# Optimization experiments

Hardware: AMD Instinct MI355X
Metric: run time of the kernel (lower is better)

## Reference

```python
import jax, jax.numpy as jnp
import numpy as np

N_NODES = 20000
N_EDGES = 320000
N_GRAPHS = 32
IN_CH = 5
HID = 64
HEADS = 4
DH = HID // HEADS  # 16
LAYERS = 8
EPS = 1e-5
SLOPE = 0.2


def setup_inputs() -> dict:
    key = jax.random.key(0)
    ks = jax.random.split(key, 32)
    inp = {}
    inp['x1'] = jax.random.normal(ks[0], (N_NODES, IN_CH), dtype=jnp.float32)
    inp['x2'] = jax.random.normal(ks[1], (N_NODES, IN_CH), dtype=jnp.float32)
    inp['edge_index1'] = jax.random.randint(ks[2], (2, N_EDGES), 0, N_NODES, dtype=jnp.int32)
    inp['edge_index2'] = jax.random.randint(ks[3], (2, N_EDGES), 0, N_NODES, dtype=jnp.int32)
    inp['batch1'] = jnp.sort(jax.random.randint(ks[4], (N_NODES,), 0, N_GRAPHS, dtype=jnp.int32))
    inp['batch2'] = jnp.sort(jax.random.randint(ks[5], (N_NODES,), 0, N_GRAPHS, dtype=jnp.int32))
    # node_lin
    inp['Wn'] = jax.random.normal(ks[6], (IN_CH, HID), dtype=jnp.float32) / np.sqrt(IN_CH)
    inp['bnode'] = jnp.zeros((HID,), dtype=jnp.float32)
    # GATv2 layers (stacked over LAYERS)
    s = 1.0 / np.sqrt(HID)
    inp['Wl'] = jax.random.normal(ks[7], (LAYERS, HID, HID), dtype=jnp.float32) * s
    inp['bl'] = jnp.zeros((LAYERS, HID), dtype=jnp.float32)
    inp['Wr'] = jax.random.normal(ks[8], (LAYERS, HID, HID), dtype=jnp.float32) * s
    inp['br'] = jnp.zeros((LAYERS, HID), dtype=jnp.float32)
    inp['att'] = jax.random.normal(ks[9], (LAYERS, HEADS, DH), dtype=jnp.float32) / np.sqrt(DH)
    inp['cbias'] = jnp.zeros((LAYERS, HID), dtype=jnp.float32)
    # batch norms
    inp['gamma'] = jnp.ones((LAYERS, HID), dtype=jnp.float32)
    inp['beta'] = jnp.zeros((LAYERS, HID), dtype=jnp.float32)
    # fc head
    inp['f1w'] = jax.random.normal(ks[10], (2 * HID, 256), dtype=jnp.float32) / np.sqrt(2 * HID)
    inp['f1b'] = jnp.zeros((256,), dtype=jnp.float32)
    inp['f2w'] = jax.random.normal(ks[11], (256, 128), dtype=jnp.float32) / np.sqrt(256)
    inp['f2b'] = jnp.zeros((128,), dtype=jnp.float32)
    inp['f3w'] = jax.random.normal(ks[12], (128, 1), dtype=jnp.float32) / np.sqrt(128)
    inp['f3b'] = jnp.zeros((1,), dtype=jnp.float32)
    return inp


def _gatv2_layer(x, src, dst, Wl, bl, Wr, br, att, bias):
    # x: [N, HID]; src/dst: [E'] (self loops included)
    N = x.shape[0]
    xl = (x @ Wl + bl).reshape(N, HEADS, DH)  # source transform
    xr = (x @ Wr + br).reshape(N, HEADS, DH)  # target transform
    e = jax.nn.leaky_relu(xl[src] + xr[dst], SLOPE)          # [E, H, DH]
    score = jnp.einsum('ehd,hd->eh', e, att)                  # [E, H]
    smax = jax.ops.segment_max(score, dst, num_segments=N)    # [N, H]
    ex = jnp.exp(score - smax[dst])
    denom = jax.ops.segment_sum(ex, dst, num_segments=N)
    alpha = ex / denom[dst]                                   # [E, H]
    msg = alpha[:, :, None] * xl[src]                         # [E, H, DH]
    out = jax.ops.segment_sum(msg, dst, num_segments=N)       # [N, H, DH]
    return out.reshape(N, HID) + bias


def _forward_once(x, edge_index, batch, Wn, bnode, Wl, bl, Wr, br, att, cbias, gamma, beta):
    N = x.shape[0]
    loop = jnp.arange(N, dtype=edge_index.dtype)
    src = jnp.concatenate([edge_index[0], loop])  # add_self_loops=True
    dst = jnp.concatenate([edge_index[1], loop])
    h = x @ Wn + bnode
    for l in range(LAYERS):
        g = _gatv2_layer(h, src, dst, Wl[l], bl[l], Wr[l], br[l], att[l], cbias[l])
        mu = g.mean(axis=0)
        var = g.var(axis=0)
        g = (g - mu) / jnp.sqrt(var + EPS) * gamma[l] + beta[l]
        h = h + jax.nn.elu(g)
    # global_mean_pool
    sums = jax.ops.segment_sum(h, batch, num_segments=N_GRAPHS)
    cnt = jax.ops.segment_sum(jnp.ones((N,), dtype=h.dtype), batch, num_segments=N_GRAPHS)
    return sums / jnp.maximum(cnt, 1.0)[:, None]


def reference(x1, edge_index1, batch1, x2, edge_index2, batch2, Wn, bnode, Wl, bl, Wr, br, att, cbias, gamma, beta, f1w, f1b, f2w, f2b, f3w, f3b):
    o1 = _forward_once(x1, edge_index1, batch1, Wn, bnode, Wl, bl, Wr, br, att, cbias, gamma, beta)
    o2 = _forward_once(x2, edge_index2, batch2, Wn, bnode, Wl, bl, Wr, br, att, cbias, gamma, beta)
    c = jnp.concatenate([o1, o2], axis=1)           # [G, 128]
    h = jax.nn.relu(c @ f1w + f1b)                   # dropout = identity (eval)
    h = jax.nn.relu(h @ f2w + f2b)
    return h @ f3w + f3b                             # [G, 1]
```

## Files before the change

### kernel.cpp

```cpp
#include <hip/hip_runtime.h>
#include <hip/hip_bf16.h>
#include <hip/hip_fp16.h>

#define N_NODES 20000
#define HID 64
#define EPS 1e-5f

typedef _Float16 h2 __attribute__((ext_vector_type(2)));

struct GP {
    const int* ei;
    const int* batch;
    const float* x;
    int* deg;
    int* cursor;
    int* csr;
    float* h;
    __half* xlh;
    __half* xrh;
    float* gb;
    float* stats;
    float* osum;
};


__global__ void k_csr_init(GP a, GP b, int n, int two) {
    int t = blockIdx.x * blockDim.x + threadIdx.x;
    if (t < n) {
        a.deg[t] = 1;
        if (two) b.deg[t] = 1;
    }
}

__global__ void k_count(GP a, GP b, int Ea, int Eb, int two) {
    int t = blockIdx.x * blockDim.x + threadIdx.x;
    if (t < Ea) atomicAdd(&a.deg[a.ei[Ea + t]], 1);
    if (two && t < Eb) atomicAdd(&b.deg[b.ei[Eb + t]], 1);
}

#define SCAN_T 1024
#define SCAN_C 20
__global__ __launch_bounds__(1024) void k_scan(GP a, GP b, int n, int totA, int totB) {
    GP g = blockIdx.x ? b : a;
    int total = blockIdx.x ? totB : totA;
    __shared__ int sd[SCAN_T];
    int t = threadIdx.x;
    int base = t * SCAN_C;
    int loc[SCAN_C];
    int s = 0;
#pragma unroll
    for (int i = 0; i < SCAN_C; ++i) {
        int idx = base + i;
        loc[i] = (idx < n) ? g.deg[idx] : 0;
        s += loc[i];
    }
    sd[t] = s;
    __syncthreads();
    for (int off = 1; off < SCAN_T; off <<= 1) {
        int v = (t >= off) ? sd[t - off] : 0;
        __syncthreads();
        sd[t] += v;
        __syncthreads();
    }
    int run = sd[t] - s;
#pragma unroll
    for (int i = 0; i < SCAN_C; ++i) {
        int idx = base + i;
        if (idx < n) { g.deg[idx] = run; g.cursor[idx] = run; run += loc[i]; }
    }
    if (t == 0) g.deg[n] = total;
}

__global__ void k_scatter(GP a, GP b, int Ea, int Eb, int n, int two) {
    int t = blockIdx.x * blockDim.x + threadIdx.x;
    if (t < Ea) {
        int s = a.ei[t], d = a.ei[Ea + t];
        a.csr[atomicAdd(&a.cursor[d], 1)] = s * 128;
    } else if (t < Ea + n) {
        int nn = t - Ea;
        a.csr[atomicAdd(&a.cursor[nn], 1)] = nn * 128;
    }
    if (two) {
        if (t < Eb) {
            int s = b.ei[t], d = b.ei[Eb + t];
            b.csr[atomicAdd(&b.cursor[d], 1)] = s * 128;
        } else if (t < Eb + n) {
            int nn = t - Eb;
            b.csr[atomicAdd(&b.cursor[nn], 1)] = nn * 128;
        }
    }
}


__global__ void k_nodelin(GP a, GP b, int nPer, const float* __restrict__ Wn,
                          const float* __restrict__ bn, int n) {
    int bid = blockIdx.x;
    GP g = a;
    if (bid >= nPer) { g = b; bid -= nPer; }
    int idx = bid * 256 + threadIdx.x;
    if (idx >= n * HID) return;
    int node = idx >> 6, c = idx & 63;
    float acc = bn[c];
#pragma unroll
    for (int k = 0; k < 5; ++k) acc += g.x[node * 5 + k] * Wn[k * HID + c];
    g.h[idx] = acc;
}


__global__ __launch_bounds__(256) void k_lin2(GP ga, GP gbp, int nPer, int n,
        const float* __restrict__ Wl, const float* __restrict__ bl,
        const float* __restrict__ Wr, const float* __restrict__ br,
        const float* __restrict__ gamma, const float* __restrict__ beta, int layer) {
    __shared__ float wls[4096], wrs[4096];
    __shared__ float hs[2048];
    int bid = blockIdx.x;
    GP g = ga;
    if (bid >= nPer) { g = gbp; bid -= nPer; }
    {
        const float4* wl4 = (const float4*)Wl;
        const float4* wr4 = (const float4*)Wr;
        float4* l4 = (float4*)wls;
        float4* r4 = (float4*)wrs;
        for (int i = threadIdx.x; i < 1024; i += 256) { l4[i] = wl4[i]; r4[i] = wr4[i]; }
    }
    int c = threadIdx.x & 63;
    int wid = threadIdx.x >> 6;
    float blv = bl[c], brv = br[c];
    float mu = 0.f, inv = 1.f, gam = 1.f, bet = 0.f;
    if (layer > 0) {
        const float* st = g.stats + (layer - 1) * 128;
        float invn = 1.0f / (float)n;
        mu = st[c] * invn;
        float var = st[64 + c] * invn - mu * mu;
        inv = rsqrtf(fmaxf(var, 0.f) + EPS);
        gam = gamma[c]; bet = beta[c];
    }
    __syncthreads();
    float* hw = &hs[wid * 512];
    const float4* hw4 = (const float4*)hw;
    for (int base = bid * 32; base < n; base += nPer * 32) {
        int nb = base + wid * 8;
        size_t off0 = (size_t)nb * 64 + c;
        float hv[8];
        if (layer > 0) {
#pragma unroll
            for (int j = 0; j < 8; ++j) {
                float gv = g.gb[off0 + j * 64];
                float ov = g.h[off0 + j * 64];
                float v = (gv - mu) * inv * gam + bet;
                v = v > 0.f ? v : expm1f(v);
                hv[j] = ov + v;
                g.h[off0 + j * 64] = hv[j];
            }
        } else {
#pragma unroll
            for (int j = 0; j < 8; ++j) hv[j] = g.h[off0 + j * 64];
        }
#pragma unroll
        for (int j = 0; j < 8; ++j) hw[j * 64 + c] = hv[j];
        float accl[8], accr[8];
#pragma unroll
        for (int j = 0; j < 8; ++j) { accl[j] = blv; accr[j] = brv; }
        for (int k4 = 0; k4 < 16; ++k4) {
            float4 hq[8];
#pragma unroll
            for (int j = 0; j < 8; ++j) hq[j] = hw4[j * 16 + k4];
#pragma unroll
            for (int kk = 0; kk < 4; ++kk) {
                float wl = wls[(k4 * 4 + kk) * 64 + c];
                float wr = wrs[(k4 * 4 + kk) * 64 + c];
#pragma unroll
                for (int j = 0; j < 8; ++j) {
                    float hx = (&hq[j].x)[kk];
                    accl[j] = fmaf(hx, wl, accl[j]);
                    accr[j] = fmaf(hx, wr, accr[j]);
                }
            }
        }
#pragma unroll
        for (int j = 0; j < 8; ++j) {
            g.xlh[off0 + j * 64] = __float2half(accl[j]);
            g.xrh[off0 + j * 64] = __float2half(accr[j]);
        }
    }
}


__device__ __forceinline__ float red8(float p) {
    p += __int_as_float(__builtin_amdgcn_update_dpp(0, __float_as_int(p), 0xB1, 0xF, 0xF, true));
    p += __int_as_float(__builtin_amdgcn_update_dpp(0, __float_as_int(p), 0x4E, 0xF, 0xF, true));
    p += __int_as_float(__builtin_amdgcn_update_dpp(0, __float_as_int(p), 0x141, 0xF, 0xF, true));
    return p;
}

__global__ __launch_bounds__(1024) void k_attn(GP ga, GP gbp, int nPer,
        const float* __restrict__ att, const float* __restrict__ cbias, int layer, int n) {
    int bid = blockIdx.x;
    GP g = (bid & 1) ? gbp : ga;
    bid >>= 1;
    int lane = threadIdx.x & 63;
    int wid = threadIdx.x >> 6;
    int hh = lane >> 5;
    int cl = lane & 31;
    int gw = bid * 16 + wid;
    int nw = nPer * 16;
    const float LOG2E = 1.44269504f;
    float a0 = att[2 * cl] * LOG2E;
    float a1 = att[2 * cl + 1] * LOG2E;
    float cb0 = cbias[2 * cl], cb1 = cbias[2 * cl + 1];
    const h2 slope = {(_Float16)0.2f, (_Float16)0.2f};
    const int* __restrict__ rowptr = g.deg;
    const int* __restrict__ csr = g.csr;
    const char* xlb = (const char*)g.xlh + (size_t)cl * 4;
    const char* xrb = (const char*)g.xrh + (size_t)cl * 4;
    float* __restrict__ gbuf = g.gb;
    float* st = g.stats + layer * 128;
    float bs0 = 0.f, bs1 = 0.f, bq0 = 0.f, bq1 = 0.f;
    for (int node = gw; node < n; node += nw) {
        int start = rowptr[node], end = rowptr[node + 1];
        h2 xrv = *(const h2*)(xrb + (size_t)node * 128);
        float sself;
        {
            h2 xs = *(const h2*)(xlb + (size_t)node * 128);
            h2 t = xs + xrv;
            h2 lk = __builtin_elementwise_max(t, t * slope);
            float sp = fmaf((float)lk.x, a0, (float)lk.y * a1);
            sself = red8(sp);
        }
        float lsum = 0.f, acc0 = 0.f, acc1 = 0.f;
        int idx = start;
        for (; idx + 8 <= end; idx += 8) {
            int off[4];
            h2 xv[4];
#pragma unroll
            for (int j = 0; j < 4; ++j) off[j] = csr[idx + 2 * j + hh];
#pragma unroll
            for (int j = 0; j < 4; ++j) xv[j] = *(const h2*)(xlb + off[j]);
#pragma unroll
            for (int j = 0; j < 4; ++j) {
                h2 t = xv[j] + xrv;
                h2 lk = __builtin_elementwise_max(t, t * slope);
                float sp = fmaf((float)lk.x, a0, (float)lk.y * a1);
                float w = exp2f(fminf(red8(sp) - sself, 110.f));
                lsum += w;
                acc0 = fmaf(w, (float)xv[j].x, acc0);
                acc1 = fmaf(w, (float)xv[j].y, acc1);
            }
        }
        for (; idx < end; idx += 2) {
            int e = idx + hh;
            bool valid = e < end;
            int off = csr[valid ? e : end - 1];
            h2 xv = *(const h2*)(xlb + off);
            h2 t = xv + xrv;
            h2 lk = __builtin_elementwise_max(t, t * slope);
            float sp = fmaf((float)lk.x, a0, (float)lk.y * a1);
            float w = exp2f(fminf(red8(sp) - sself, 110.f));
            w = valid ? w : 0.f;
            lsum += w;
            acc0 = fmaf(w, (float)xv.x, acc0);
            acc1 = fmaf(w, (float)xv.y, acc1);
        }
        lsum += __shfl_xor(lsum, 32);
        acc0 += __shfl_xor(acc0, 32);
        acc1 += __shfl_xor(acc1, 32);
        if (hh == 0) {
            float invl = 1.0f / lsum;
            float o0 = acc0 * invl + cb0;
            float o1 = acc1 * invl + cb1;
            float2 o = {o0, o1};
            *(float2*)(gbuf + (size_t)node * 64 + 2 * cl) = o;
            bs0 += o0; bs1 += o1;
            bq0 += o0 * o0; bq1 += o1 * o1;
        }
    }
    __shared__ float2 sred[1024];
    float2 z = {0.f, 0.f};
    float2 v1 = {bs0, bs1};
    sred[threadIdx.x] = (hh == 0) ? v1 : z;
    __syncthreads();
    if (threadIdx.x < 32) {
        float t0 = 0.f, t1 = 0.f;
#pragma unroll
        for (int w = 0; w < 16; ++w) { float2 s = sred[w * 64 + threadIdx.x]; t0 += s.x; t1 += s.y; }
        atomicAdd(&st[2 * threadIdx.x], t0);
        atomicAdd(&st[2 * threadIdx.x + 1], t1);
    }
    __syncthreads();
    float2 v2 = {bq0, bq1};
    sred[threadIdx.x] = (hh == 0) ? v2 : z;
    __syncthreads();
    if (threadIdx.x < 32) {
        float t0 = 0.f, t1 = 0.f;
#pragma unroll
        for (int w = 0; w < 16; ++w) { float2 s = sred[w * 64 + threadIdx.x]; t0 += s.x; t1 += s.y; }
        atomicAdd(&st[64 + 2 * threadIdx.x], t0);
        atomicAdd(&st[64 + 2 * threadIdx.x + 1], t1);
    }
}


__global__ __launch_bounds__(256) void k_pool(GP ga, GP gbp, int nPer,
        const float* __restrict__ gamma, const float* __restrict__ beta, int n) {
    int bid = blockIdx.x;
    GP g = ga;
    if (bid >= nPer) { g = gbp; bid -= nPer; }
    int lane = threadIdx.x & 63, w = threadIdx.x >> 6;
    const float* st = g.stats + 7 * 128;
    float invn = 1.f / (float)n;
    float mu = st[lane] * invn;
    float var = st[64 + lane] * invn - mu * mu;
    float inv = rsqrtf(fmaxf(var, 0.f) + EPS);
    float gam = gamma[lane], bet = beta[lane];
    int chunk = (n + nPer - 1) / nPer;
    int s = bid * chunk;
    int e = min(s + chunk, n);
    float acc = 0.f;
    int cur = -1;
    for (int node = s + w; node < e; node += 4) {
        int bg = g.batch[node];
        size_t off = (size_t)node * 64 + lane;
        float gv = g.gb[off];
        float hv = g.h[off];
        float v = (gv - mu) * inv * gam + bet;
        float hn = hv + (v > 0.f ? v : expm1f(v));
        if (bg != cur) {
            if (cur >= 0) atomicAdd(&g.osum[cur * 64 + lane], acc);
            acc = 0.f; cur = bg;
        }
        acc += hn;
    }
    if (cur >= 0) atomicAdd(&g.osum[cur * 64 + lane], acc);
}


__device__ __forceinline__ int lb(const int* __restrict__ b, int n, int v) {
    int lo = 0, hi = n;
    while (lo < hi) { int mid = (lo + hi) >> 1; if (b[mid] < v) lo = mid + 1; else hi = mid; }
    return lo;
}

__global__ __launch_bounds__(256) void k_fc(const float* __restrict__ o1, const float* __restrict__ o2,
                                            const int* __restrict__ b1, const int* __restrict__ b2,
                                            const float* __restrict__ f1w, const float* __restrict__ f1b,
                                            const float* __restrict__ f2w, const float* __restrict__ f2b,
                                            const float* __restrict__ f3w, const float* __restrict__ f3b,
                                            float* __restrict__ out, int n) {
    int gid = blockIdx.x, t = threadIdx.x;
    __shared__ float cin[128];
    __shared__ float h1[256];
    __shared__ float red[128];
    __shared__ int cnts[2];
    if (t == 0) cnts[0] = lb(b1, n, gid + 1) - lb(b1, n, gid);
    if (t == 1) cnts[1] = lb(b2, n, gid + 1) - lb(b2, n, gid);
    __syncthreads();
    if (t < 64) {
        float c1 = (float)(cnts[0] > 0 ? cnts[0] : 1);
        float c2 = (float)(cnts[1] > 0 ? cnts[1] : 1);
        cin[t] = o1[gid * 64 + t] / c1;
        cin[64 + t] = o2[gid * 64 + t] / c2;
    }
    __syncthreads();
    float a = f1b[t];
#pragma unroll 8
    for (int k = 0; k < 128; ++k) a += cin[k] * f1w[k * 256 + t];
    h1[t] = fmaxf(a, 0.f);
    __syncthreads();
    if (t < 128) {
        float a2 = f2b[t];
#pragma unroll 8
        for (int k = 0; k < 256; ++k) a2 += h1[k] * f2w[k * 128 + t];
        red[t] = fmaxf(a2, 0.f) * f3w[t];
    }
    __syncthreads();
    for (int off = 64; off > 0; off >>= 1) {
        if (t < off) red[t] += red[t + off];
        __syncthreads();
    }
    if (t == 0) out[gid] = red[0] + f3b[0];
}


extern "C" void kernel_launch(void* const* d_in, const int* in_sizes, int n_in,
                              void* d_out, int out_size, void* d_ws, size_t ws_size,
                              hipStream_t stream) {
    const float* x1 = (const float*)d_in[0];
    const float* x2 = (const float*)d_in[1];
    const int* ei1 = (const int*)d_in[2];
    const int* ei2 = (const int*)d_in[3];
    const int* b1 = (const int*)d_in[4];
    const int* b2 = (const int*)d_in[5];
    const float* Wn = (const float*)d_in[6];
    const float* bnode = (const float*)d_in[7];
    const float* Wl = (const float*)d_in[8];
    const float* bl = (const float*)d_in[9];
    const float* Wr = (const float*)d_in[10];
    const float* br = (const float*)d_in[11];
    const float* att = (const float*)d_in[12];
    const float* cbias = (const float*)d_in[13];
    const float* gamma = (const float*)d_in[14];
    const float* beta = (const float*)d_in[15];
    const float* f1w = (const float*)d_in[16];
    const float* f1b = (const float*)d_in[17];
    const float* f2w = (const float*)d_in[18];
    const float* f2b = (const float*)d_in[19];
    const float* f3w = (const float*)d_in[20];
    const float* f3b = (const float*)d_in[21];
    float* out = (float*)d_out;

    const int N = N_NODES;
    const int EA = in_sizes[2] / 2;
    const int EB = in_sizes[3] / 2;
    const size_t INT_PG = 20096 + 20096 + 340096;
    const size_t BIG = (size_t)N * 64;
    const size_t SMALL = 2 * 1024 + 2 * 2048;
    const size_t dualBytes = 2 * INT_PG * 4 + (8 * BIG + SMALL) * 4;
    const int dual = (ws_size >= dualBytes) ? 1 : 0;

    int* ibase = (int*)d_ws;
    int* iA = ibase;
    int* iB = dual ? ibase + INT_PG : ibase;
    float* fbase = (float*)(ibase + (size_t)(dual ? 2 : 1) * INT_PG);
    float* hA = fbase;
    float* xlA = hA + BIG;
    float* xrA = xlA + BIG;
    float* gbA = xrA + BIG;
    float* hB = dual ? gbA + BIG : hA;
    float* xlB = dual ? hB + BIG : xlA;
    float* xrB = dual ? xlB + BIG : xrA;
    float* gbB = dual ? xrB + BIG : gbA;
    float* small = dual ? gbB + BIG : gbA + BIG;
    float* statsA = small;
    float* statsB = small + 1024;
    float* osumA = small + 2048;
    float* osumB = small + 4096;

    GP A, B;
    A.ei = ei1; A.batch = b1; A.x = x1;
    A.deg = iA; A.cursor = iA + 20096; A.csr = iA + 40192;
    A.h = hA; A.xlh = (__half*)xlA; A.xrh = (__half*)xrA;
    A.gb = gbA; A.stats = statsA; A.osum = osumA;
    B.ei = ei2; B.batch = b2; B.x = x2;
    B.deg = iB; B.cursor = iB + 20096; B.csr = iB + 40192;
    B.h = hB; B.xlh = (__half*)xlB; B.xrh = (__half*)xrB;
    B.gb = gbB; B.stats = statsB; B.osum = osumB;

    hipMemsetAsync(small, 0, SMALL * sizeof(float), stream);

    const int LIN2_NB = 320;
    const int ATT_NB = 256;
    const int POOL_NB = 250;

    if (dual) {
        int Emax = EA > EB ? EA : EB;
        k_csr_init<<<(N + 255) / 256, 256, 0, stream>>>(A, B, N, 1);
        k_count<<<(Emax + 255) / 256, 256, 0, stream>>>(A, B, EA, EB, 1);
        k_scan<<<2, 1024, 0, stream>>>(A, B, N, EA + N, EB + N);
        k_scatter<<<(Emax + N + 255) / 256, 256, 0, stream>>>(A, B, EA, EB, N, 1);
        k_nodelin<<<2 * ((N * 64) / 256), 256, 0, stream>>>(A, B, (N * 64) / 256, Wn, bnode, N);
        for (int l = 0; l < 8; ++l) {
            const float* gm = l ? gamma + (l - 1) * 64 : gamma;
            const float* bt = l ? beta + (l - 1) * 64 : beta;
            k_lin2<<<2 * LIN2_NB, 256, 0, stream>>>(A, B, LIN2_NB, N, Wl + l * 4096, bl + l * 64,
                                                    Wr + l * 4096, br + l * 64, gm, bt, l);
            k_attn<<<2 * ATT_NB, 1024, 0, stream>>>(A, B, ATT_NB, att + l * 64, cbias + l * 64, l, N);
        }
        k_pool<<<2 * POOL_NB, 256, 0, stream>>>(A, B, POOL_NB, gamma + 7 * 64, beta + 7 * 64, N);
    } else {
        for (int gi = 0; gi < 2; ++gi) {
            GP G = gi ? B : A;
            int E = gi ? EB : EA;
            k_csr_init<<<(N + 255) / 256, 256, 0, stream>>>(G, G, N, 0);
            k_count<<<(E + 255) / 256, 256, 0, stream>>>(G, G, E, E, 0);
            k_scan<<<1, 1024, 0, stream>>>(G, G, N, E + N, E + N);
            k_scatter<<<(E + N + 255) / 256, 256, 0, stream>>>(G, G, E, E, N, 0);
            k_nodelin<<<(N * 64) / 256, 256, 0, stream>>>(G, G, (N * 64) / 256, Wn, bnode, N);
            for (int l = 0; l < 8; ++l) {
                const float* gm = l ? gamma + (l - 1) * 64 : gamma;
                const float* bt = l ? beta + (l - 1) * 64 : beta;
                k_lin2<<<LIN2_NB, 256, 0, stream>>>(G, G, LIN2_NB, N, Wl + l * 4096, bl + l * 64,
                                                    Wr + l * 4096, br + l * 64, gm, bt, l);
                k_attn<<<2 * ATT_NB, 1024, 0, stream>>>(G, G, ATT_NB, att + l * 64, cbias + l * 64, l, N);
            }
            k_pool<<<POOL_NB, 256, 0, stream>>>(G, G, POOL_NB, gamma + 7 * 64, beta + 7 * 64, N);
        }
    }
    k_fc<<<32, 256, 0, stream>>>(osumA, osumB, b1, b2, f1w, f1b, f2w, f2b, f3w, f3b, out, N);
}
```

Measured before the change: 660.5 us.

## Use fp16 dot2 for linear transforms and 16-lane-per-edge attention

```diff
diff --git a/kernel.cpp b/kernel.cpp
--- a/kernel.cpp
+++ b/kernel.cpp
@@ -1,12 +1,15 @@
 #include <hip/hip_runtime.h>
 #include <hip/hip_bf16.h>
 #include <hip/hip_fp16.h>
+#include <stdint.h>
 
 #define N_NODES 20000
 #define HID 64
 #define EPS 1e-5f
 
 typedef _Float16 h2 __attribute__((ext_vector_type(2)));
+
+__device__ __forceinline__ h2 u2h(uint32_t u) { union { uint32_t u; h2 h; } v; v.u = u; return v.h; }
 
 struct GP {
     const int* ei;
@@ -92,6 +95,26 @@
 }
 
 
+__global__ void k_wcvt(const float* __restrict__ Wl, const float* __restrict__ Wr,
+                       uint32_t* __restrict__ wpk) {
+    int t = blockIdx.x * 256 + threadIdx.x;
+    if (t >= 16384) return;
+    int l = t >> 11, r = t & 2047;
+    int k2 = r >> 6, c = r & 63;
+    const float* wl = Wl + l * 4096;
+    const float* wr = Wr + l * 4096;
+    h2 a, b;
+    a.x = (_Float16)wl[(2 * k2) * 64 + c];
+    a.y = (_Float16)wl[(2 * k2 + 1) * 64 + c];
+    b.x = (_Float16)wr[(2 * k2) * 64 + c];
+    b.y = (_Float16)wr[(2 * k2 + 1) * 64 + c];
+    union { h2 h; uint32_t u; } ua, ub;
+    ua.h = a; ub.h = b;
+    wpk[l * 4096 + r] = ua.u;
+    wpk[l * 4096 + 2048 + r] = ub.u;
+}
+
+
 __global__ void k_nodelin(GP a, GP b, int nPer, const float* __restrict__ Wn,
                           const float* __restrict__ bn, int n) {
     int bid = blockIdx.x;
@@ -108,20 +131,18 @@
 
 
 __global__ __launch_bounds__(256) void k_lin2(GP ga, GP gbp, int nPer, int n,
-        const float* __restrict__ Wl, const float* __restrict__ bl,
-        const float* __restrict__ Wr, const float* __restrict__ br,
+        const uint32_t* __restrict__ wl2g, const float* __restrict__ bl,
+        const uint32_t* __restrict__ wr2g, const float* __restrict__ br,
         const float* __restrict__ gamma, const float* __restrict__ beta, int layer) {
-    __shared__ float wls[4096], wrs[4096];
-    __shared__ float hs[2048];
+    __shared__ uint32_t wl2[2048], wr2[2048];
+    __shared__ _Float16 hs16[2048];
     int bid = blockIdx.x;
     GP g = ga;
     if (bid >= nPer) { g = gbp; bid -= nPer; }
     {
-        const float4* wl4 = (const float4*)Wl;
-        const float4* wr4 = (const float4*)Wr;
-        float4* l4 = (float4*)wls;
-        float4* r4 = (float4*)wrs;
-        for (int i = threadIdx.x; i < 1024; i += 256) { l4[i] = wl4[i]; r4[i] = wr4[i]; }
+        uint4* dl = (uint4*)wl2; const uint4* sl = (const uint4*)wl2g;
+        uint4* dr = (uint4*)wr2; const uint4* sr = (const uint4*)wr2g;
+        for (int i = threadIdx.x; i < 512; i += 256) { dl[i] = sl[i]; dr[i] = sr[i]; }
     }
     int c = threadIdx.x & 63;
     int wid = threadIdx.x >> 6;
@@ -135,61 +156,58 @@
         inv = rsqrtf(fmaxf(var, 0.f) + EPS);
         gam = gamma[c]; bet = beta[c];
     }
-    __syncthreads();
-    float* hw = &hs[wid * 512];
-    const float4* hw4 = (const float4*)hw;
-    for (int base = bid * 32; base < n; base += nPer * 32) {
-        int nb = base + wid * 8;
-        size_t off0 = (size_t)nb * 64 + c;
-        float hv[8];
-        if (layer > 0) {
+    int nb = bid * 32 + wid * 8;
+    size_t off0 = (size_t)nb * 64 + c;
+    float hv[8];
+    if (layer > 0) {
+#pragma unroll
+        for (int j = 0; j < 8; ++j) {
+            float gv = g.gb[off0 + j * 64];
+            float ov = g.h[off0 + j * 64];
+            float v = (gv - mu) * inv * gam + bet;
+            v = v > 0.f ? v : expm1f(v);
+            hv[j] = ov + v;
+            g.h[off0 + j * 64] = hv[j];
+        }
+    } else {
+#pragma unroll
+        for (int j = 0; j < 8; ++j) hv[j] = g.h[off0 + j * 64];
+    }
+    _Float16* hw16 = &hs16[wid * 512];
+#pragma unroll
+    for (int j = 0; j < 8; ++j) hw16[j * 64 + c] = (_Float16)hv[j];
+    __syncthreads();
+    const uint32_t* hw2 = (const uint32_t*)hw16;
+    float accl[8], accr[8];
+#pragma unroll
+    for (int j = 0; j < 8; ++j) { accl[j] = blv; accr[j] = brv; }
+    for (int k8 = 0; k8 < 8; ++k8) {
+        uint4 hq[8];
+#pragma unroll
+        for (int j = 0; j < 8; ++j) hq[j] = *(const uint4*)&hw2[j * 32 + k8 * 4];
+#pragma unroll
+        for (int p = 0; p < 4; ++p) {
+            h2 wlv = u2h(wl2[(k8 * 4 + p) * 64 + c]);
+            h2 wrv = u2h(wr2[(k8 * 4 + p) * 64 + c]);
 #pragma unroll
             for (int j = 0; j < 8; ++j) {
-                float gv = g.gb[off0 + j * 64];
-                float ov = g.h[off0 + j * 64];
-                float v = (gv - mu) * inv * gam + bet;
-                v = v > 0.f ? v : expm1f(v);
-                hv[j] = ov + v;
-                g.h[off0 + j * 64] = hv[j];
+                h2 hp = u2h((&hq[j].x)[p]);
+                accl[j] = __builtin_amdgcn_fdot2(hp, wlv, accl[j], false);
+                accr[j] = __builtin_amdgcn_fdot2(hp, wrv, accr[j], false);
             }
-        } else {
-#pragma unroll
-            for (int j = 0; j < 8; ++j) hv[j] = g.h[off0 + j * 64];
-        }
-#pragma unroll
-        for (int j = 0; j < 8; ++j) hw[j * 64 + c] = hv[j];
-        float accl[8], accr[8];
-#pragma unroll
-        for (int j = 0; j < 8; ++j) { accl[j] = blv; accr[j] = brv; }
-        for (int k4 = 0; k4 < 16; ++k4) {
-            float4 hq[8];
-#pragma unroll
-            for (int j = 0; j < 8; ++j) hq[j] = hw4[j * 16 + k4];
-#pragma unroll
-            for (int kk = 0; kk < 4; ++kk) {
-                float wl = wls[(k4 * 4 + kk) * 64 + c];
-                float wr = wrs[(k4 * 4 + kk) * 64 + c];
-#pragma unroll
-                for (int j = 0; j < 8; ++j) {
-                    float hx = (&hq[j].x)[kk];
-                    accl[j] = fmaf(hx, wl, accl[j]);
-                    accr[j] = fmaf(hx, wr, accr[j]);
-                }
-            }
-        }
-#pragma unroll
-        for (int j = 0; j < 8; ++j) {
-            g.xlh[off0 + j * 64] = __float2half(accl[j]);
-            g.xrh[off0 + j * 64] = __float2half(accr[j]);
-        }
-    }
-}
-
-
-__device__ __forceinline__ float red8(float p) {
+        }
+    }
+#pragma unroll
+    for (int j = 0; j < 8; ++j) {
+        g.xlh[off0 + j * 64] = __float2half(accl[j]);
+        g.xrh[off0 + j * 64] = __float2half(accr[j]);
+    }
+}
+
+
+__device__ __forceinline__ float red4(float p) {
     p += __int_as_float(__builtin_amdgcn_update_dpp(0, __float_as_int(p), 0xB1, 0xF, 0xF, true));
     p += __int_as_float(__builtin_amdgcn_update_dpp(0, __float_as_int(p), 0x4E, 0xF, 0xF, true));
-    p += __int_as_float(__builtin_amdgcn_update_dpp(0, __float_as_int(p), 0x141, 0xF, 0xF, true));
     return p;
 }
 
@@ -200,102 +218,148 @@
     bid >>= 1;
     int lane = threadIdx.x & 63;
     int wid = threadIdx.x >> 6;
-    int hh = lane >> 5;
-    int cl = lane & 31;
+    int slot = lane >> 4;
+    int cl = lane & 15;
     int gw = bid * 16 + wid;
     int nw = nPer * 16;
-    const float LOG2E = 1.44269504f;
-    float a0 = att[2 * cl] * LOG2E;
-    float a1 = att[2 * cl + 1] * LOG2E;
-    float cb0 = cbias[2 * cl], cb1 = cbias[2 * cl + 1];
+    const float L2E = 1.44269504f;
+    h2 ap0, ap1;
+    ap0.x = (_Float16)(att[4 * cl] * L2E);
+    ap0.y = (_Float16)(att[4 * cl + 1] * L2E);
+    ap1.x = (_Float16)(att[4 * cl + 2] * L2E);
+    ap1.y = (_Float16)(att[4 * cl + 3] * L2E);
+    float cb0 = cbias[4 * cl], cb1 = cbias[4 * cl + 1];
+    float cb2 = cbias[4 * cl + 2], cb3 = cbias[4 * cl + 3];
     const h2 slope = {(_Float16)0.2f, (_Float16)0.2f};
     const int* __restrict__ rowptr = g.deg;
     const int* __restrict__ csr = g.csr;
-    const char* xlb = (const char*)g.xlh + (size_t)cl * 4;
-    const char* xrb = (const char*)g.xrh + (size_t)cl * 4;
+    const char* xlb = (const char*)g.xlh + (size_t)cl * 8;
+    const char* xrb = (const char*)g.xrh + (size_t)cl * 8;
     float* __restrict__ gbuf = g.gb;
     float* st = g.stats + layer * 128;
-    float bs0 = 0.f, bs1 = 0.f, bq0 = 0.f, bq1 = 0.f;
+    float bs0 = 0.f, bs1 = 0.f, bs2 = 0.f, bs3 = 0.f;
+    float bq0 = 0.f, bq1 = 0.f, bq2 = 0.f, bq3 = 0.f;
     for (int node = gw; node < n; node += nw) {
         int start = rowptr[node], end = rowptr[node + 1];
-        h2 xrv = *(const h2*)(xrb + (size_t)node * 128);
+        uint2 xru = *(const uint2*)(xrb + (size_t)node * 128);
+        h2 xr0 = u2h(xru.x), xr1 = u2h(xru.y);
         float sself;
         {
-            h2 xs = *(const h2*)(xlb + (size_t)node * 128);
-            h2 t = xs + xrv;
-            h2 lk = __builtin_elementwise_max(t, t * slope);
-            float sp = fmaf((float)lk.x, a0, (float)lk.y * a1);
-            sself = red8(sp);
-        }
-        float lsum = 0.f, acc0 = 0.f, acc1 = 0.f;
+            uint2 xsu = *(const uint2*)(xlb + (size_t)node * 128);
+            h2 t0 = u2h(xsu.x) + xr0, t1 = u2h(xsu.y) + xr1;
+            h2 l0 = __builtin_elementwise_max(t0, t0 * slope);
+            h2 l1 = __builtin_elementwise_max(t1, t1 * slope);
+            float sp = __builtin_amdgcn_fdot2(l1, ap1,
+                       __builtin_amdgcn_fdot2(l0, ap0, 0.f, false), false);
+            sself = red4(sp);
+        }
+        float lsum = 0.f, a0 = 0.f, a1 = 0.f, a2 = 0.f, a3 = 0.f;
         int idx = start;
         for (; idx + 8 <= end; idx += 8) {
-            int off[4];
-            h2 xv[4];
-#pragma unroll
-            for (int j = 0; j < 4; ++j) off[j] = csr[idx + 2 * j + hh];
-#pragma unroll
-            for (int j = 0; j < 4; ++j) xv[j] = *(const h2*)(xlb + off[j]);
-#pragma unroll
-            for (int j = 0; j < 4; ++j) {
-                h2 t = xv[j] + xrv;
-                h2 lk = __builtin_elementwise_max(t, t * slope);
-                float sp = fmaf((float)lk.x, a0, (float)lk.y * a1);
-                float w = exp2f(fminf(red8(sp) - sself, 110.f));
+            int o0 = csr[idx + slot], o1 = csr[idx + 4 + slot];
+            uint2 xu0 = *(const uint2*)(xlb + o0);
+            uint2 xu1 = *(const uint2*)(xlb + o1);
+#pragma unroll
+            for (int q = 0; q < 2; ++q) {
+                uint2 xu = q ? xu1 : xu0;
+                h2 v0 = u2h(xu.x), v1 = u2h(xu.y);
+                h2 t0 = v0 + xr0, t1 = v1 + xr1;
+                h2 l0 = __builtin_elementwise_max(t0, t0 * slope);
+                h2 l1 = __builtin_elementwise_max(t1, t1 * slope);
+                float sp = __builtin_amdgcn_fdot2(l1, ap1,
+                           __builtin_amdgcn_fdot2(l0, ap0, 0.f, false), false);
+                float w = exp2f(fminf(red4(sp) - sself, 110.f));
                 lsum += w;
-                acc0 = fmaf(w, (float)xv[j].x, acc0);
-                acc1 = fmaf(w, (float)xv[j].y, acc1);
+                a0 = fmaf(w, (float)v0.x, a0);
+                a1 = fmaf(w, (float)v0.y, a1);
+                a2 = fmaf(w, (float)v1.x, a2);
+                a3 = fmaf(w, (float)v1.y, a3);
             }
         }
-        for (; idx < end; idx += 2) {
-            int e = idx + hh;
+        for (; idx + 4 <= end; idx += 4) {
+            int o = csr[idx + slot];
+            uint2 xu = *(const uint2*)(xlb + o);
+            h2 v0 = u2h(xu.x), v1 = u2h(xu.y);
+            h2 t0 = v0 + xr0, t1 = v1 + xr1;
+            h2 l0 = __builtin_elementwise_max(t0, t0 * slope);
+            h2 l1 = __builtin_elementwise_max(t1, t1 * slope);
+            float sp = __builtin_amdgcn_fdot2(l1, ap1,
+                       __builtin_amdgcn_fdot2(l0, ap0, 0.f, false), false);
+            float w = exp2f(fminf(red4(sp) - sself, 110.f));
+            lsum += w;
+            a0 = fmaf(w, (float)v0.x, a0);
+            a1 = fmaf(w, (float)v0.y, a1);
+            a2 = fmaf(w, (float)v1.x, a2);
+            a3 = fmaf(w, (float)v1.y, a3);
+        }
+        if (idx < end) {
+            int e = idx + slot;
             bool valid = e < end;
-            int off = csr[valid ? e : end - 1];
-            h2 xv = *(const h2*)(xlb + off);
-            h2 t = xv + xrv;
-            h2 lk = __builtin_elementwise_max(t, t * slope);
-            float sp = fmaf((float)lk.x, a0, (float)lk.y * a1);
-            float w = exp2f(fminf(red8(sp) - sself, 110.f));
+            int o = csr[valid ? e : end - 1];
+            uint2 xu = *(const uint2*)(xlb + o);
+            h2 v0 = u2h(xu.x), v1 = u2h(xu.y);
+            h2 t0 = v0 + xr0, t1 = v1 + xr1;
+            h2 l0 = __builtin_elementwise_max(t0, t0 * slope);
+            h2 l1 = __builtin_elementwise_max(t1, t1 * slope);
+            float sp = __builtin_amdgcn_fdot2(l1, ap1,
+                       __builtin_amdgcn_fdot2(l0, ap0, 0.f, false), false);
+            float w = exp2f(fminf(red4(sp) - sself, 110.f));
             w = valid ? w : 0.f;
             lsum += w;
-            acc0 = fmaf(w, (float)xv.x, acc0);
-            acc1 = fmaf(w, (float)xv.y, acc1);
-        }
-        lsum += __shfl_xor(lsum, 32);
-        acc0 += __shfl_xor(acc0, 32);
-        acc1 += __shfl_xor(acc1, 32);
-        if (hh == 0) {
+            a0 = fmaf(w, (float)v0.x, a0);
+            a1 = fmaf(w, (float)v0.y, a1);
+            a2 = fmaf(w, (float)v1.x, a2);
+            a3 = fmaf(w, (float)v1.y, a3);
+        }
+        lsum += __shfl_xor(lsum, 16); lsum += __shfl_xor(lsum, 32);
+        a0 += __shfl_xor(a0, 16); a0 += __shfl_xor(a0, 32);
+        a1 += __shfl_xor(a1, 16); a1 += __shfl_xor(a1, 32);
+        a2 += __shfl_xor(a2, 16); a2 += __shfl_xor(a2, 32);
+        a3 += __shfl_xor(a3, 16); a3 += __shfl_xor(a3, 32);
+        if (slot == 0) {
             float invl = 1.0f / lsum;
-            float o0 = acc0 * invl + cb0;
-            float o1 = acc1 * invl + cb1;
-            float2 o = {o0, o1};
-            *(float2*)(gbuf + (size_t)node * 64 + 2 * cl) = o;
-            bs0 += o0; bs1 += o1;
-            bq0 += o0 * o0; bq1 += o1 * o1;
-        }
-    }
-    __shared__ float2 sred[1024];
-    float2 z = {0.f, 0.f};
-    float2 v1 = {bs0, bs1};
-    sred[threadIdx.x] = (hh == 0) ? v1 : z;
-    __syncthreads();
-    if (threadIdx.x < 32) {
-        float t0 = 0.f, t1 = 0.f;
-#pragma unroll
-        for (int w = 0; w < 16; ++w) { float2 s = sred[w * 64 + threadIdx.x]; t0 += s.x; t1 += s.y; }
-        atomicAdd(&st[2 * threadIdx.x], t0);
-        atomicAdd(&st[2 * threadIdx.x + 1], t1);
-    }
-    __syncthreads();
-    float2 v2 = {bq0, bq1};
-    sred[threadIdx.x] = (hh == 0) ? v2 : z;
-    __syncthreads();
-    if (threadIdx.x < 32) {
-        float t0 = 0.f, t1 = 0.f;
-#pragma unroll
-        for (int w = 0; w < 16; ++w) { float2 s = sred[w * 64 + threadIdx.x]; t0 += s.x; t1 += s.y; }
-        atomicAdd(&st[64 + 2 * threadIdx.x], t0);
-        atomicAdd(&st[64 + 2 * threadIdx.x + 1], t1);
+            float o0 = a0 * invl + cb0;
+            float o1 = a1 * invl + cb1;
+            float o2 = a2 * invl + cb2;
+            float o3 = a3 * invl + cb3;
+            float4 o = {o0, o1, o2, o3};
+            *(float4*)(gbuf + (size_t)node * 64 + 4 * cl) = o;
+            bs0 += o0; bs1 += o1; bs2 += o2; bs3 += o3;
+            bq0 += o0 * o0; bq1 += o1 * o1; bq2 += o2 * o2; bq3 += o3 * o3;
+        }
+    }
+    __shared__ float4 sred[1024];
+    float4 z = {0.f, 0.f, 0.f, 0.f};
+    float4 s1 = {bs0, bs1, bs2, bs3};
+    sred[threadIdx.x] = (slot == 0) ? s1 : z;
+    __syncthreads();
+    if (threadIdx.x < 16) {
+        float t0 = 0.f, t1 = 0.f, t2 = 0.f, t3 = 0.f;
+#pragma unroll
+        for (int w = 0; w < 16; ++w) {
+            float4 s = sred[w * 64 + threadIdx.x];
+            t0 += s.x; t1 += s.y; t2 += s.z; t3 += s.w;
+        }
+        atomicAdd(&st[4 * threadIdx.x], t0);
+        atomicAdd(&st[4 * threadIdx.x + 1], t1);
+        atomicAdd(&st[4 * threadIdx.x + 2], t2);
+        atomicAdd(&st[4 * threadIdx.x + 3], t3);
+    }
+    __syncthreads();
+    float4 s2 = {bq0, bq1, bq2, bq3};
+    sred[threadIdx.x] = (slot == 0) ? s2 : z;
+    __syncthreads();
+    if (threadIdx.x < 16) {
+        float t0 = 0.f, t1 = 0.f, t2 = 0.f, t3 = 0.f;
+#pragma unroll
+        for (int w = 0; w < 16; ++w) {
+            float4 s = sred[w * 64 + threadIdx.x];
+            t0 += s.x; t1 += s.y; t2 += s.z; t3 += s.w;
+        }
+        atomicAdd(&st[64 + 4 * threadIdx.x], t0);
+        atomicAdd(&st[64 + 4 * threadIdx.x + 1], t1);
+        atomicAdd(&st[64 + 4 * threadIdx.x + 2], t2);
+        atomicAdd(&st[64 + 4 * threadIdx.x + 3], t3);
     }
 }
 
@@ -414,7 +478,8 @@
     const size_t INT_PG = 20096 + 20096 + 340096;
     const size_t BIG = (size_t)N * 64;
     const size_t SMALL = 2 * 1024 + 2 * 2048;
-    const size_t dualBytes = 2 * INT_PG * 4 + (8 * BIG + SMALL) * 4;
+    const size_t WPK = 32768;
+    const size_t dualBytes = 2 * INT_PG * 4 + (8 * BIG + SMALL + WPK) * 4;
     const int dual = (ws_size >= dualBytes) ? 1 : 0;
 
     int* ibase = (int*)d_ws;
@@ -434,6 +499,7 @@
     float* statsB = small + 1024;
     float* osumA = small + 2048;
     float* osumB = small + 4096;
+    uint32_t* wpk = (uint32_t*)(small + SMALL);
 
     GP A, B;
     A.ei = ei1; A.batch = b1; A.x = x1;
@@ -447,7 +513,7 @@
 
     hipMemsetAsync(small, 0, SMALL * sizeof(float), stream);
 
-    const int LIN2_NB = 320;
+    const int LIN2_NB = 625;
     const int ATT_NB = 256;
     const int POOL_NB = 250;
 
@@ -457,12 +523,14 @@
         k_count<<<(Emax + 255) / 256, 256, 0, stream>>>(A, B, EA, EB, 1);
         k_scan<<<2, 1024, 0, stream>>>(A, B, N, EA + N, EB + N);
         k_scatter<<<(Emax + N + 255) / 256, 256, 0, stream>>>(A, B, EA, EB, N, 1);
+        k_wcvt<<<64, 256, 0, stream>>>(Wl, Wr, wpk);
         k_nodelin<<<2 * ((N * 64) / 256), 256, 0, stream>>>(A, B, (N * 64) / 256, Wn, bnode, N);
         for (int l = 0; l < 8; ++l) {
             const float* gm = l ? gamma + (l - 1) * 64 : gamma;
             const float* bt = l ? beta + (l - 1) * 64 : beta;
-            k_lin2<<<2 * LIN2_NB, 256, 0, stream>>>(A, B, LIN2_NB, N, Wl + l * 4096, bl + l * 64,
-                                                    Wr + l * 4096, br + l * 64, gm, bt, l);
+            k_lin2<<<2 * LIN2_NB, 256, 0, stream>>>(A, B, LIN2_NB, N,
+                                                    wpk + l * 4096, bl + l * 64,
+                                                    wpk + l * 4096 + 2048, br + l * 64, gm, bt, l);
             k_attn<<<2 * ATT_NB, 1024, 0, stream>>>(A, B, ATT_NB, att + l * 64, cbias + l * 64, l, N);
         }
         k_pool<<<2 * POOL_NB, 256, 0, stream>>>(A, B, POOL_NB, gamma + 7 * 64, beta + 7 * 64, N);
@@ -474,12 +542,14 @@
             k_count<<<(E + 255) / 256, 256, 0, stream>>>(G, G, E, E, 0);
             k_scan<<<1, 1024, 0, stream>>>(G, G, N, E + N, E + N);
             k_scatter<<<(E + N + 255) / 256, 256, 0, stream>>>(G, G, E, E, N, 0);
+            if (gi == 0) k_wcvt<<<64, 256, 0, stream>>>(Wl, Wr, wpk);
             k_nodelin<<<(N * 64) / 256, 256, 0, stream>>>(G, G, (N * 64) / 256, Wn, bnode, N);
             for (int l = 0; l < 8; ++l) {
                 const float* gm = l ? gamma + (l - 1) * 64 : gamma;
                 const float* bt = l ? beta + (l - 1) * 64 : beta;
-                k_lin2<<<LIN2_NB, 256, 0, stream>>>(G, G, LIN2_NB, N, Wl + l * 4096, bl + l * 64,
-                                                    Wr + l * 4096, br + l * 64, gm, bt, l);
+                k_lin2<<<LIN2_NB, 256, 0, stream>>>(G, G, LIN2_NB, N,
+                                                    wpk + l * 4096, bl + l * 64,
+                                                    wpk + l * 4096 + 2048, br + l * 64, gm, bt, l);
                 k_attn<<<2 * ATT_NB, 1024, 0, stream>>>(G, G, ATT_NB, att + l * 64, cbias + l * 64, l, N);
             }
             k_pool<<<POOL_NB, 256, 0, stream>>>(G, G, POOL_NB, gamma + 7 * 64, beta + 7 * 64, N);
```

Measured after the change: 766.8 us. 1.16x slower.
